# Kernel optimization log

Measured on AMD Instinct MI355X. Metric: run time of the kernel, lower is better.

## Reference

```python
import jax, jax.numpy as jnp
import numpy as np

WIN = (2, 6, 12)            # (vert, lat, lon) window size
P = WIN[0] * WIN[1] * WIN[2]  # 144 patches per window
DIM = 192
HEADS = 6
TYPE_OF_WINDOWS = 4 * 16     # ceil(8/2) * ceil(96/6)
N_WINDOWS = 4 * 16 * 15      # 960 (batch = 1)
BIAS_ROWS = (2 * WIN[2] - 1) * WIN[1] * WIN[1] * WIN[0] * WIN[0]  # 3312


def _construct_index():
    """Replicates EarthAttention3DAbsolute._construct_index in numpy."""
    wz, wh, ww = WIN
    coords_zi = np.arange(wz)
    coords_zj = -np.arange(wz) * wz
    coords_hi = np.arange(wh)
    coords_hj = -np.arange(wh) * wh
    coords_w = np.arange(ww)
    c1 = np.stack(np.meshgrid(coords_zi, coords_hi, coords_w, indexing='ij')).reshape(3, -1)
    c2 = np.stack(np.meshgrid(coords_zj, coords_hj, coords_w, indexing='ij')).reshape(3, -1)
    coords = (c1[:, :, None] - c2[:, None, :]).transpose(1, 2, 0)  # (P, P, 3)
    coords[:, :, 2] += ww - 1
    coords[:, :, 1] *= 2 * ww - 1
    coords[:, :, 0] *= (2 * ww - 1) * wh * wh
    return coords.sum(-1).reshape(-1).astype(np.int32)  # (P*P,)


def setup_inputs() -> dict:
    key = jax.random.key(0)
    ks = jax.random.split(key, 8)
    x = jax.random.normal(ks[0], (N_WINDOWS, P, DIM), dtype=jnp.float32)
    mask = jax.random.normal(ks[1], (N_WINDOWS, P, P), dtype=jnp.float32)
    W_qkv = jax.random.normal(ks[2], (DIM, 3 * DIM), dtype=jnp.float32) * (DIM ** -0.5)
    b_qkv = jax.random.normal(ks[3], (3 * DIM,), dtype=jnp.float32) * 0.02
    W_out = jax.random.normal(ks[4], (DIM, DIM), dtype=jnp.float32) * (DIM ** -0.5)
    b_out = jax.random.normal(ks[5], (DIM,), dtype=jnp.float32) * 0.02
    bias_table = jax.random.normal(ks[6], (BIAS_ROWS, TYPE_OF_WINDOWS, HEADS), dtype=jnp.float32) * 0.02
    position_index = jnp.asarray(_construct_index())
    return {"x": x, "mask": mask, "W_qkv": W_qkv, "b_qkv": b_qkv,
            "W_out": W_out, "b_out": b_out, "bias_table": bias_table,
            "position_index": position_index}


def reference(x, mask, W_qkv, b_qkv, W_out, b_out, bias_table, position_index):
    NW, Pn, C = x.shape            # (960, 144, 192)
    H = HEADS
    D = C // H
    scale = D ** -0.5
    T = bias_table.shape[1]        # type_of_windows

    # QKV projection -> (3, NW, H, P, D)
    qkv = (x @ W_qkv + b_qkv).reshape(NW, Pn, 3, H, D).transpose(2, 0, 3, 1, 4)
    q, k, v = qkv[0] * scale, qkv[1], qkv[2]

    # per-window scores (NW, H, P, P)
    attn = jnp.einsum('whpd,whqd->whpq', q, k)

    # gathered absolute position bias -> (T, H, P, P)
    bias = bias_table[position_index].reshape(Pn, Pn, T, H).transpose(2, 3, 0, 1)
    attn = (attn.reshape(-1, T, H, Pn, Pn) + bias[None]).reshape(NW, H, Pn, Pn)

    # additive shift mask (n_windows, P, P), batch-broadcast
    nwin = mask.shape[0]
    attn = (attn.reshape(NW // nwin, nwin, H, Pn, Pn) + mask[None, :, None]).reshape(NW, H, Pn, Pn)

    attn = jax.nn.softmax(attn, axis=-1)

    out = jnp.einsum('whpq,whqd->wphd', attn, v).reshape(NW, Pn, C)
    return out @ W_out + b_out
```

## Files before the change

### kernel.cpp

```cpp
#include <hip/hip_runtime.h>

#define NWIN   960
#define PP     144
#define CC     192
#define HH     6
#define DD     32
#define TT     64
#define PQ     (PP*PP)
#define MROWS  (NWIN*PP)
#define NQKV   576
#define KT     48
#define QSCALE 0.17677669529663687f


__global__ __launch_bounds__(256) void k0_bias_expand(
    const float* __restrict__ table, const int* __restrict__ pidx,
    float* __restrict__ bias_ws)
{
    int pq = blockIdx.x * 256 + threadIdx.x;
    int idx = pidx[pq];
    const float* row = table + (long)idx * 384;
    for (int th = 0; th < 384; ++th) {
        bias_ws[(unsigned)th * PQ + pq] = row[th];
    }
}

__global__ __launch_bounds__(256) void k2_fused(
    const float* __restrict__ x, const float* __restrict__ Wqkv,
    const float* __restrict__ bqkv, const float* __restrict__ mask,
    const float* __restrict__ bias_ws, float* __restrict__ ao)
{
    __shared__ float Qs[DD][PP + 1];
    __shared__ float Ks[DD][KT + 1];
    __shared__ float Vs[KT][DD];
    __shared__ float UN[6912];

    const int tid = threadIdx.x;
    const int wh = blockIdx.x;
    const int w = wh / HH;
    const int h = wh % HH;
    const int th = (w % TT) * HH + h;
    const float* xw = x + (long)w * PP * CC;
    const float* mb = mask + (long)w * PQ;
    const float* bb = bias_ws + (long)th * PQ;

    const int tp = tid >> 4;
    const int tq = tid & 15;
    const int p0 = tp * 9;
    const int q0 = tq * 3;
    const int d0 = tq * 2;

    {
        float qacc[9][2];
#pragma unroll
        for (int i = 0; i < 9; ++i) { qacc[i][0] = 0.f; qacc[i][1] = 0.f; }

        for (int kc = 0; kc < CC; kc += 32) {
            float* Xs = UN;
            float* Wq = UN + 4752;
            __syncthreads();
            for (int idx = tid; idx < 1152; idx += 256) {
                int p = idx >> 3;
                int cq = (idx & 7) * 4;
                float4 g = *(const float4*)&xw[(long)p * CC + kc + cq];
                Xs[p * 33 + cq + 0] = g.x; Xs[p * 33 + cq + 1] = g.y;
                Xs[p * 33 + cq + 2] = g.z; Xs[p * 33 + cq + 3] = g.w;
            }
            {
                int r = tid >> 3;
                int cq = (tid & 7) * 4;
                float4 g = *(const float4*)&Wqkv[(long)(kc + r) * NQKV + h * DD + cq];
                Wq[r * 33 + cq + 0] = g.x; Wq[r * 33 + cq + 1] = g.y;
                Wq[r * 33 + cq + 2] = g.z; Wq[r * 33 + cq + 3] = g.w;
            }
            __syncthreads();
            for (int c = 0; c < 32; ++c) {
                float b0 = Wq[c * 33 + d0];
                float b1 = Wq[c * 33 + d0 + 1];
                float a[9];
#pragma unroll
                for (int i = 0; i < 9; ++i) a[i] = Xs[(p0 + i) * 33 + c];
#pragma unroll
                for (int i = 0; i < 9; ++i) {
                    qacc[i][0] = fmaf(a[i], b0, qacc[i][0]);
                    qacc[i][1] = fmaf(a[i], b1, qacc[i][1]);
                }
            }
        }
        float bq0 = bqkv[h * DD + d0], bq1 = bqkv[h * DD + d0 + 1];
#pragma unroll
        for (int i = 0; i < 9; ++i) {
            Qs[d0 + 0][p0 + i] = (qacc[i][0] + bq0) * QSCALE;
            Qs[d0 + 1][p0 + i] = (qacc[i][1] + bq1) * QSCALE;
        }
    }

    float O[9][2];
    float mrun[9], lrun[9];
#pragma unroll
    for (int i = 0; i < 9; ++i) {
        O[i][0] = 0.f; O[i][1] = 0.f;
        mrun[i] = -INFINITY; lrun[i] = 0.f;
    }

    const int ty = tid >> 4;
    const int tx = tid & 15;

    for (int kt = 0; kt < 3; ++kt) {
        const int qoff = kt * KT;

        float kv[3][4];
#pragma unroll
        for (int i = 0; i < 3; ++i)
#pragma unroll
            for (int j = 0; j < 4; ++j) kv[i][j] = 0.f;

        for (int kc = 0; kc < CC; kc += 32) {
            float* Xs2 = UN;
            float* Wkv = UN + 1584;
            __syncthreads();
            for (int idx = tid; idx < 384; idx += 256) {
                int r = idx >> 3;
                int cq = (idx & 7) * 4;
                float4 g = *(const float4*)&xw[(long)(qoff + r) * CC + kc + cq];
                Xs2[r * 33 + cq + 0] = g.x; Xs2[r * 33 + cq + 1] = g.y;
                Xs2[r * 33 + cq + 2] = g.z; Xs2[r * 33 + cq + 3] = g.w;
            }
            for (int idx = tid; idx < 512; idx += 256) {
                int r = idx >> 4;
                int q8 = idx & 15;
                int col  = (q8 < 8) ? (192 + h * DD + q8 * 4)
                                    : (384 + h * DD + (q8 - 8) * 4);
                int lcol = q8 * 4;
                float4 g = *(const float4*)&Wqkv[(long)(kc + r) * NQKV + col];
                *(float4*)&Wkv[r * 64 + lcol] = g;
            }
            __syncthreads();
            for (int c = 0; c < 32; ++c) {
                float a2[3];
#pragma unroll
                for (int i = 0; i < 3; ++i) a2[i] = Xs2[(ty * 3 + i) * 33 + c];
                float4 b4 = *(float4*)&Wkv[c * 64 + tx * 4];
#pragma unroll
                for (int i = 0; i < 3; ++i) {
                    kv[i][0] = fmaf(a2[i], b4.x, kv[i][0]);
                    kv[i][1] = fmaf(a2[i], b4.y, kv[i][1]);
                    kv[i][2] = fmaf(a2[i], b4.z, kv[i][2]);
                    kv[i][3] = fmaf(a2[i], b4.w, kv[i][3]);
                }
            }
        }
        __syncthreads();

        if (tx < 8) {
            int dc = tx * 4;
            float4 bk = *(const float4*)&bqkv[192 + h * DD + dc];
#pragma unroll
            for (int i = 0; i < 3; ++i) {
                int r = ty * 3 + i;
                Ks[dc + 0][r] = kv[i][0] + bk.x;
                Ks[dc + 1][r] = kv[i][1] + bk.y;
                Ks[dc + 2][r] = kv[i][2] + bk.z;
                Ks[dc + 3][r] = kv[i][3] + bk.w;
            }
        } else {
            int dc = tx * 4 - 32;
            float4 bv = *(const float4*)&bqkv[384 + h * DD + dc];
#pragma unroll
            for (int i = 0; i < 3; ++i) {
                int r = ty * 3 + i;
                float4 o;
                o.x = kv[i][0] + bv.x; o.y = kv[i][1] + bv.y;
                o.z = kv[i][2] + bv.z; o.w = kv[i][3] + bv.w;
                *(float4*)&Vs[r][dc] = o;
            }
        }
        __syncthreads();

        float acc[9][3];
#pragma unroll
        for (int i = 0; i < 9; ++i)
#pragma unroll
            for (int j = 0; j < 3; ++j) acc[i][j] = 0.f;

        for (int d = 0; d < DD; ++d) {
            float a[9], b[3];
#pragma unroll
            for (int i = 0; i < 9; ++i) a[i] = Qs[d][p0 + i];
#pragma unroll
            for (int j = 0; j < 3; ++j) b[j] = Ks[d][q0 + j];
#pragma unroll
            for (int i = 0; i < 9; ++i)
#pragma unroll
                for (int j = 0; j < 3; ++j) acc[i][j] = fmaf(a[i], b[j], acc[i][j]);
        }

        float* Ps = UN;
        float tmax[9];
#pragma unroll
        for (int i = 0; i < 9; ++i) {
            tmax[i] = -INFINITY;
            int pp = p0 + i;
#pragma unroll
            for (int j = 0; j < 3; ++j) {
                int qq = qoff + q0 + j;
                float s = acc[i][j] + bb[pp * PP + qq] + mb[pp * PP + qq];
                acc[i][j] = s;
                tmax[i] = fmaxf(tmax[i], s);
            }
        }
#pragma unroll
        for (int i = 0; i < 9; ++i) {
#pragma unroll
            for (int off = 1; off < 16; off <<= 1)
                tmax[i] = fmaxf(tmax[i], __shfl_xor(tmax[i], off, 16));
        }
#pragma unroll
        for (int i = 0; i < 9; ++i) {
            float mnew = fmaxf(mrun[i], tmax[i]);
            float scal = __expf(mrun[i] - mnew);
            float psum = 0.f;
#pragma unroll
            for (int j = 0; j < 3; ++j) {
                float p = __expf(acc[i][j] - mnew);
                Ps[(p0 + i) * KT + q0 + j] = p;
                psum += p;
            }
#pragma unroll
            for (int off = 1; off < 16; off <<= 1)
                psum += __shfl_xor(psum, off, 16);
            lrun[i] = lrun[i] * scal + psum;
            O[i][0] *= scal; O[i][1] *= scal;
            mrun[i] = mnew;
        }
        __syncthreads();

        for (int qq = 0; qq < KT; ++qq) {
            float2 v2 = *(const float2*)&Vs[qq][d0];
#pragma unroll
            for (int i = 0; i < 9; ++i) {
                float p = Ps[(p0 + i) * KT + qq];
                O[i][0] = fmaf(p, v2.x, O[i][0]);
                O[i][1] = fmaf(p, v2.y, O[i][1]);
            }
        }
    }

#pragma unroll
    for (int i = 0; i < 9; ++i) {
        float inv = 1.f / lrun[i];
        float2 o2; o2.x = O[i][0] * inv; o2.y = O[i][1] * inv;
        *(float2*)&ao[((long)(w * PP + p0 + i)) * CC + h * DD + d0] = o2;
    }
}

#define BM 128
#define BN 64
#define KC 64
__global__ __launch_bounds__(256) void k3_proj(
    const float* __restrict__ ain, const float* __restrict__ Wout,
    const float* __restrict__ bout, float* __restrict__ out)
{
    __shared__ float As[BM][KC + 1];
    __shared__ float Bs[KC][BN];

    const int tid = threadIdx.x;
    const int rowBase = blockIdx.x * BM;
    const int colBase = blockIdx.y * BN;
    const int r0 = (tid >> 4) * 8;
    const int c0 = (tid & 15) * 4;

    float acc[8][4];
#pragma unroll
    for (int i = 0; i < 8; ++i)
#pragma unroll
        for (int j = 0; j < 4; ++j) acc[i][j] = 0.f;

    for (int kc = 0; kc < CC; kc += KC) {
#pragma unroll
        for (int it = 0; it < 8; ++it) {
            int idx = tid + it * 256;
            int row = idx >> 4;
            int kq  = (idx & 15) * 4;
            float4 g = *(const float4*)&ain[(long)(rowBase + row) * CC + kc + kq];
            As[row][kq + 0] = g.x; As[row][kq + 1] = g.y;
            As[row][kq + 2] = g.z; As[row][kq + 3] = g.w;
        }
#pragma unroll
        for (int it = 0; it < 4; ++it) {
            int idx = tid + it * 256;
            int kk = idx >> 4;
            int n0 = (idx & 15) * 4;
            float4 g = *(const float4*)&Wout[(long)(kc + kk) * CC + colBase + n0];
            *(float4*)&Bs[kk][n0] = g;
        }
        __syncthreads();

        for (int kk = 0; kk < KC; ++kk) {
            float4 b4 = *(const float4*)&Bs[kk][c0];
            float a[8];
#pragma unroll
            for (int i = 0; i < 8; ++i) a[i] = As[r0 + i][kk];
#pragma unroll
            for (int i = 0; i < 8; ++i) {
                acc[i][0] = fmaf(a[i], b4.x, acc[i][0]);
                acc[i][1] = fmaf(a[i], b4.y, acc[i][1]);
                acc[i][2] = fmaf(a[i], b4.z, acc[i][2]);
                acc[i][3] = fmaf(a[i], b4.w, acc[i][3]);
            }
        }
        __syncthreads();
    }

    const int c = colBase + c0;
    float b0 = bout[c], b1 = bout[c + 1], b2 = bout[c + 2], b3 = bout[c + 3];
#pragma unroll
    for (int i = 0; i < 8; ++i) {
        int m = rowBase + r0 + i;
        float4 o;
        o.x = acc[i][0] + b0; o.y = acc[i][1] + b1;
        o.z = acc[i][2] + b2; o.w = acc[i][3] + b3;
        *(float4*)&out[(long)m * CC + c] = o;
    }
}

extern "C" void kernel_launch(void* const* d_in, const int* in_sizes, int n_in,
                              void* d_out, int out_size, void* d_ws, size_t ws_size,
                              hipStream_t stream) {
    const float* x     = (const float*)d_in[0];
    const float* mask  = (const float*)d_in[1];
    const float* Wqkv  = (const float*)d_in[2];
    const float* bqkv  = (const float*)d_in[3];
    const float* Wout  = (const float*)d_in[4];
    const float* bout  = (const float*)d_in[5];
    const float* btab  = (const float*)d_in[6];
    const int*   pidx  = (const int*)d_in[7];
    float* out = (float*)d_out;
    float* ws  = (float*)d_ws;

    float* bws = out;
    float* ao  = ws;

    hipLaunchKernelGGL(k0_bias_expand, dim3(81), dim3(256), 0, stream,
                       btab, pidx, bws);
    hipLaunchKernelGGL(k2_fused, dim3(NWIN * HH), dim3(256), 0, stream,
                       x, Wqkv, bqkv, mask, bws, ao);
    hipLaunchKernelGGL(k3_proj, dim3(MROWS / BM, CC / BN), dim3(256), 0, stream,
                       ao, Wout, bout, out);
}
```

Before: 1.519 ms.

## Rewrite fused attention kernel with split-bf16 MFMA matrix instructions

```diff
diff --git a/kernel.cpp b/kernel.cpp
--- a/kernel.cpp
+++ b/kernel.cpp
@@ -1,4 +1,5 @@
 #include <hip/hip_runtime.h>
+#include <hip/hip_bf16.h>
 
 #define NWIN   960
 #define PP     144
@@ -9,9 +10,54 @@
 #define PQ     (PP*PP)
 #define MROWS  (NWIN*PP)
 #define NQKV   576
-#define KT     48
 #define QSCALE 0.17677669529663687f
 
+using f32x4 = __attribute__((ext_vector_type(4))) float;
+using s16x8 = __attribute__((ext_vector_type(8))) short;
+
+__device__ inline unsigned short f2bf(float x) {
+    __hip_bfloat16 b = __float2bfloat16(x);
+    return *reinterpret_cast<unsigned short*>(&b);
+}
+__device__ inline float bf2f(unsigned short u) {
+    __hip_bfloat16 b = *reinterpret_cast<__hip_bfloat16*>(&u);
+    return __bfloat162float(b);
+}
+__device__ inline unsigned pack_hl(float x) {
+    unsigned short hi = f2bf(x);
+    unsigned short lo = f2bf(x - bf2f(hi));
+    return ((unsigned)lo << 16) | (unsigned)hi;
+}
+
+struct FragHL { s16x8 hi; s16x8 lo; };
+
+__device__ inline FragHL load_frag_hl(const unsigned* base, int row0, int stride) {
+    int lane = threadIdx.x & 63;
+    const unsigned* p = base + (row0 + (lane & 15)) * stride + 8 * (lane >> 4);
+    FragHL f;
+#pragma unroll
+    for (int j = 0; j < 8; ++j) {
+        unsigned u = p[j];
+        f.hi[j] = (short)(u & 0xffffu);
+        f.lo[j] = (short)(u >> 16);
+    }
+    return f;
+}
+__device__ inline s16x8 load_frag_bf(const unsigned short* base, int row0,
+                                     int stride, int koff) {
+    int lane = threadIdx.x & 63;
+    const unsigned short* p = base + (row0 + (lane & 15)) * stride + koff + 8 * (lane >> 4);
+    s16x8 f;
+#pragma unroll
+    for (int j = 0; j < 8; ++j) f[j] = (short)p[j];
+    return f;
+}
+__device__ inline f32x4 mfma3(const FragHL& a, const FragHL& b, f32x4 c) {
+    c = __builtin_amdgcn_mfma_f32_16x16x32_bf16(a.hi, b.hi, c, 0, 0, 0);
+    c = __builtin_amdgcn_mfma_f32_16x16x32_bf16(a.hi, b.lo, c, 0, 0, 0);
+    c = __builtin_amdgcn_mfma_f32_16x16x32_bf16(a.lo, b.hi, c, 0, 0, 0);
+    return c;
+}
 
 __global__ __launch_bounds__(256) void k0_bias_expand(
     const float* __restrict__ table, const int* __restrict__ pidx,
@@ -25,232 +71,194 @@
     }
 }
 
-__global__ __launch_bounds__(256) void k2_fused(
+__global__ __launch_bounds__(256) void k2_mfma(
     const float* __restrict__ x, const float* __restrict__ Wqkv,
     const float* __restrict__ bqkv, const float* __restrict__ mask,
     const float* __restrict__ bias_ws, float* __restrict__ ao)
 {
-    __shared__ float Qs[DD][PP + 1];
-    __shared__ float Ks[DD][KT + 1];
-    __shared__ float Vs[KT][DD];
-    __shared__ float UN[6912];
-
-    const int tid = threadIdx.x;
-    const int wh = blockIdx.x;
-    const int w = wh / HH;
-    const int h = wh % HH;
-    const int th = (w % TT) * HH + h;
+    __shared__ __align__(16) char LDSBUF[63744];
+    unsigned*       Qs = (unsigned*)(LDSBUF);
+    unsigned*       Ks = (unsigned*)(LDSBUF + 20736);
+    unsigned short* Vt = (unsigned short*)(LDSBUF + 41472);
+    unsigned short* Ps = (unsigned short*)(LDSBUF + 52224);
+    unsigned*       Xs = (unsigned*)(LDSBUF);
+    unsigned*       Wt = (unsigned*)(LDSBUF + 20736);
+
+    const int tid  = threadIdx.x;
+    const int lane = tid & 63;
+    const int wv   = tid >> 6;
+    const int bid = blockIdx.x;
+    const int wh  = (bid & 7) * 720 + (bid >> 3);
+    const int w = wh / HH, h = wh % HH;
+    const int thh = (w % TT) * HH + h;
     const float* xw = x + (long)w * PP * CC;
     const float* mb = mask + (long)w * PQ;
-    const float* bb = bias_ws + (long)th * PQ;
-
-    const int tp = tid >> 4;
-    const int tq = tid & 15;
-    const int p0 = tp * 9;
-    const int q0 = tq * 3;
-    const int d0 = tq * 2;
+    const float* bb = bias_ws + (long)thh * PQ;
+
+    const int nmt = (wv == 0) ? 3 : 2;
+    int mts[3];
+    mts[0] = wv; mts[1] = wv + 4; mts[2] = 8;
+
+    const int lgrp = lane >> 4;
+    const int l15  = lane & 15;
+
+    f32x4 acc1[3][6];
+#pragma unroll
+    for (int i = 0; i < 3; ++i)
+#pragma unroll
+        for (int n = 0; n < 6; ++n) acc1[i][n] = f32x4{0.f, 0.f, 0.f, 0.f};
+
+    for (int kc = 0; kc < CC; kc += 32) {
+        __syncthreads();
+        for (int idx = tid; idx < 1152; idx += 256) {
+            int p  = idx >> 3;
+            int c4 = (idx & 7) * 4;
+            float4 g = *(const float4*)&xw[p * CC + kc + c4];
+            unsigned* dst = Xs + p * 36 + c4;
+            dst[0] = pack_hl(g.x); dst[1] = pack_hl(g.y);
+            dst[2] = pack_hl(g.z); dst[3] = pack_hl(g.w);
+        }
+        for (int idx = tid; idx < 768; idx += 256) {
+            int k  = idx / 24;
+            int n4 = (idx % 24) * 4;
+            int seg = n4 >> 5;
+            int gcol = seg * 192 + h * DD + (n4 & 31);
+            float4 g = *(const float4*)&Wqkv[(long)(kc + k) * NQKV + gcol];
+            Wt[(n4 + 0) * 36 + k] = pack_hl(g.x);
+            Wt[(n4 + 1) * 36 + k] = pack_hl(g.y);
+            Wt[(n4 + 2) * 36 + k] = pack_hl(g.z);
+            Wt[(n4 + 3) * 36 + k] = pack_hl(g.w);
+        }
+        __syncthreads();
+        FragHL bfr[6];
+#pragma unroll
+        for (int nt = 0; nt < 6; ++nt) bfr[nt] = load_frag_hl(Wt, nt * 16, 36);
+        for (int im = 0; im < nmt; ++im) {
+            FragHL a = load_frag_hl(Xs, mts[im] * 16, 36);
+#pragma unroll
+            for (int nt = 0; nt < 6; ++nt)
+                acc1[im][nt] = mfma3(a, bfr[nt], acc1[im][nt]);
+        }
+    }
+    __syncthreads();
+
+    for (int im = 0; im < nmt; ++im) {
+        int mrow = mts[im] * 16 + 4 * lgrp;
+#pragma unroll
+        for (int half = 0; half < 2; ++half) {
+            int d = l15 + 16 * half;
+            float bq = bqkv[h * DD + d];
+            float bk = bqkv[192 + h * DD + d];
+            float bv = bqkv[384 + h * DD + d];
+            f32x4 q4 = acc1[im][half];
+            f32x4 k4 = acc1[im][2 + half];
+            f32x4 v4 = acc1[im][4 + half];
+#pragma unroll
+            for (int r = 0; r < 4; ++r) {
+                int row = mrow + r;
+                Qs[row * 36 + d] = pack_hl((q4[r] + bq) * QSCALE);
+                Ks[row * 36 + d] = pack_hl(k4[r] + bk);
+                Vt[d * 168 + row] = f2bf(v4[r] + bv);
+            }
+        }
+    }
+    for (int idx = tid; idx < 512; idx += 256) {
+        int d = idx >> 4;
+        Vt[d * 168 + 144 + (idx & 15)] = 0;
+    }
+    __syncthreads();
+
+    f32x4 sacc[3][9];
+#pragma unroll
+    for (int i = 0; i < 3; ++i)
+#pragma unroll
+        for (int n = 0; n < 9; ++n) sacc[i][n] = f32x4{0.f, 0.f, 0.f, 0.f};
 
     {
-        float qacc[9][2];
-#pragma unroll
-        for (int i = 0; i < 9; ++i) { qacc[i][0] = 0.f; qacc[i][1] = 0.f; }
-
-        for (int kc = 0; kc < CC; kc += 32) {
-            float* Xs = UN;
-            float* Wq = UN + 4752;
-            __syncthreads();
-            for (int idx = tid; idx < 1152; idx += 256) {
-                int p = idx >> 3;
-                int cq = (idx & 7) * 4;
-                float4 g = *(const float4*)&xw[(long)p * CC + kc + cq];
-                Xs[p * 33 + cq + 0] = g.x; Xs[p * 33 + cq + 1] = g.y;
-                Xs[p * 33 + cq + 2] = g.z; Xs[p * 33 + cq + 3] = g.w;
-            }
-            {
-                int r = tid >> 3;
-                int cq = (tid & 7) * 4;
-                float4 g = *(const float4*)&Wqkv[(long)(kc + r) * NQKV + h * DD + cq];
-                Wq[r * 33 + cq + 0] = g.x; Wq[r * 33 + cq + 1] = g.y;
-                Wq[r * 33 + cq + 2] = g.z; Wq[r * 33 + cq + 3] = g.w;
-            }
-            __syncthreads();
-            for (int c = 0; c < 32; ++c) {
-                float b0 = Wq[c * 33 + d0];
-                float b1 = Wq[c * 33 + d0 + 1];
-                float a[9];
-#pragma unroll
-                for (int i = 0; i < 9; ++i) a[i] = Xs[(p0 + i) * 33 + c];
-#pragma unroll
-                for (int i = 0; i < 9; ++i) {
-                    qacc[i][0] = fmaf(a[i], b0, qacc[i][0]);
-                    qacc[i][1] = fmaf(a[i], b1, qacc[i][1]);
+        FragHL aq[3];
+        for (int im = 0; im < nmt; ++im) aq[im] = load_frag_hl(Qs, mts[im] * 16, 36);
+        for (int nt = 0; nt < 9; ++nt) {
+            FragHL b = load_frag_hl(Ks, nt * 16, 36);
+            for (int im = 0; im < nmt; ++im)
+                sacc[im][nt] = mfma3(aq[im], b, sacc[im][nt]);
+        }
+    }
+
+    float rsum[3][4];
+    for (int im = 0; im < nmt; ++im) {
+        int prow = mts[im] * 16 + 4 * lgrp;
+#pragma unroll
+        for (int nt = 0; nt < 9; ++nt) {
+            int qcol = nt * 16 + l15;
+#pragma unroll
+            for (int r = 0; r < 4; ++r)
+                sacc[im][nt][r] += bb[(prow + r) * PP + qcol] + mb[(prow + r) * PP + qcol];
+        }
+#pragma unroll
+        for (int r = 0; r < 4; ++r) {
+            float mx = sacc[im][0][r];
+#pragma unroll
+            for (int nt = 1; nt < 9; ++nt) mx = fmaxf(mx, sacc[im][nt][r]);
+#pragma unroll
+            for (int off = 1; off < 16; off <<= 1)
+                mx = fmaxf(mx, __shfl_xor(mx, off, 16));
+            float sum = 0.f;
+#pragma unroll
+            for (int nt = 0; nt < 9; ++nt) {
+                float e = __expf(sacc[im][nt][r] - mx);
+                sacc[im][nt][r] = e;
+                sum += e;
+            }
+#pragma unroll
+            for (int off = 1; off < 16; off <<= 1)
+                sum += __shfl_xor(sum, off, 16);
+            rsum[im][r] = sum;
+        }
+    }
+
+    f32x4 oacc[3][2];
+#pragma unroll
+    for (int i = 0; i < 3; ++i) { oacc[i][0] = f32x4{0.f,0.f,0.f,0.f};
+                                  oacc[i][1] = f32x4{0.f,0.f,0.f,0.f}; }
+
+    for (int c = 0; c < 5; ++c) {
+        __syncthreads();
+        for (int im = 0; im < nmt; ++im) {
+            int prow = mts[im] * 16 + 4 * lgrp;
+#pragma unroll
+            for (int half = 0; half < 2; ++half) {
+                int nt = 2 * c + half;
+                int col = l15 + 16 * half;
+#pragma unroll
+                for (int r = 0; r < 4; ++r) {
+                    unsigned short v = (nt < 9) ? f2bf(sacc[im][nt][r]) : (unsigned short)0;
+                    Ps[(prow + r) * 40 + col] = v;
                 }
             }
         }
-        float bq0 = bqkv[h * DD + d0], bq1 = bqkv[h * DD + d0 + 1];
-#pragma unroll
-        for (int i = 0; i < 9; ++i) {
-            Qs[d0 + 0][p0 + i] = (qacc[i][0] + bq0) * QSCALE;
-            Qs[d0 + 1][p0 + i] = (qacc[i][1] + bq1) * QSCALE;
-        }
-    }
-
-    float O[9][2];
-    float mrun[9], lrun[9];
-#pragma unroll
-    for (int i = 0; i < 9; ++i) {
-        O[i][0] = 0.f; O[i][1] = 0.f;
-        mrun[i] = -INFINITY; lrun[i] = 0.f;
-    }
-
-    const int ty = tid >> 4;
-    const int tx = tid & 15;
-
-    for (int kt = 0; kt < 3; ++kt) {
-        const int qoff = kt * KT;
-
-        float kv[3][4];
-#pragma unroll
-        for (int i = 0; i < 3; ++i)
-#pragma unroll
-            for (int j = 0; j < 4; ++j) kv[i][j] = 0.f;
-
-        for (int kc = 0; kc < CC; kc += 32) {
-            float* Xs2 = UN;
-            float* Wkv = UN + 1584;
-            __syncthreads();
-            for (int idx = tid; idx < 384; idx += 256) {
-                int r = idx >> 3;
-                int cq = (idx & 7) * 4;
-                float4 g = *(const float4*)&xw[(long)(qoff + r) * CC + kc + cq];
-                Xs2[r * 33 + cq + 0] = g.x; Xs2[r * 33 + cq + 1] = g.y;
-                Xs2[r * 33 + cq + 2] = g.z; Xs2[r * 33 + cq + 3] = g.w;
-            }
-            for (int idx = tid; idx < 512; idx += 256) {
-                int r = idx >> 4;
-                int q8 = idx & 15;
-                int col  = (q8 < 8) ? (192 + h * DD + q8 * 4)
-                                    : (384 + h * DD + (q8 - 8) * 4);
-                int lcol = q8 * 4;
-                float4 g = *(const float4*)&Wqkv[(long)(kc + r) * NQKV + col];
-                *(float4*)&Wkv[r * 64 + lcol] = g;
-            }
-            __syncthreads();
-            for (int c = 0; c < 32; ++c) {
-                float a2[3];
-#pragma unroll
-                for (int i = 0; i < 3; ++i) a2[i] = Xs2[(ty * 3 + i) * 33 + c];
-                float4 b4 = *(float4*)&Wkv[c * 64 + tx * 4];
-#pragma unroll
-                for (int i = 0; i < 3; ++i) {
-                    kv[i][0] = fmaf(a2[i], b4.x, kv[i][0]);
-                    kv[i][1] = fmaf(a2[i], b4.y, kv[i][1]);
-                    kv[i][2] = fmaf(a2[i], b4.z, kv[i][2]);
-                    kv[i][3] = fmaf(a2[i], b4.w, kv[i][3]);
-                }
-            }
-        }
-        __syncthreads();
-
-        if (tx < 8) {
-            int dc = tx * 4;
-            float4 bk = *(const float4*)&bqkv[192 + h * DD + dc];
-#pragma unroll
-            for (int i = 0; i < 3; ++i) {
-                int r = ty * 3 + i;
-                Ks[dc + 0][r] = kv[i][0] + bk.x;
-                Ks[dc + 1][r] = kv[i][1] + bk.y;
-                Ks[dc + 2][r] = kv[i][2] + bk.z;
-                Ks[dc + 3][r] = kv[i][3] + bk.w;
-            }
-        } else {
-            int dc = tx * 4 - 32;
-            float4 bv = *(const float4*)&bqkv[384 + h * DD + dc];
-#pragma unroll
-            for (int i = 0; i < 3; ++i) {
-                int r = ty * 3 + i;
-                float4 o;
-                o.x = kv[i][0] + bv.x; o.y = kv[i][1] + bv.y;
-                o.z = kv[i][2] + bv.z; o.w = kv[i][3] + bv.w;
-                *(float4*)&Vs[r][dc] = o;
-            }
-        }
-        __syncthreads();
-
-        float acc[9][3];
-#pragma unroll
-        for (int i = 0; i < 9; ++i)
-#pragma unroll
-            for (int j = 0; j < 3; ++j) acc[i][j] = 0.f;
-
-        for (int d = 0; d < DD; ++d) {
-            float a[9], b[3];
-#pragma unroll
-            for (int i = 0; i < 9; ++i) a[i] = Qs[d][p0 + i];
-#pragma unroll
-            for (int j = 0; j < 3; ++j) b[j] = Ks[d][q0 + j];
-#pragma unroll
-            for (int i = 0; i < 9; ++i)
-#pragma unroll
-                for (int j = 0; j < 3; ++j) acc[i][j] = fmaf(a[i], b[j], acc[i][j]);
-        }
-
-        float* Ps = UN;
-        float tmax[9];
-#pragma unroll
-        for (int i = 0; i < 9; ++i) {
-            tmax[i] = -INFINITY;
-            int pp = p0 + i;
-#pragma unroll
-            for (int j = 0; j < 3; ++j) {
-                int qq = qoff + q0 + j;
-                float s = acc[i][j] + bb[pp * PP + qq] + mb[pp * PP + qq];
-                acc[i][j] = s;
-                tmax[i] = fmaxf(tmax[i], s);
-            }
-        }
-#pragma unroll
-        for (int i = 0; i < 9; ++i) {
-#pragma unroll
-            for (int off = 1; off < 16; off <<= 1)
-                tmax[i] = fmaxf(tmax[i], __shfl_xor(tmax[i], off, 16));
-        }
-#pragma unroll
-        for (int i = 0; i < 9; ++i) {
-            float mnew = fmaxf(mrun[i], tmax[i]);
-            float scal = __expf(mrun[i] - mnew);
-            float psum = 0.f;
-#pragma unroll
-            for (int j = 0; j < 3; ++j) {
-                float p = __expf(acc[i][j] - mnew);
-                Ps[(p0 + i) * KT + q0 + j] = p;
-                psum += p;
-            }
-#pragma unroll
-            for (int off = 1; off < 16; off <<= 1)
-                psum += __shfl_xor(psum, off, 16);
-            lrun[i] = lrun[i] * scal + psum;
-            O[i][0] *= scal; O[i][1] *= scal;
-            mrun[i] = mnew;
-        }
-        __syncthreads();
-
-        for (int qq = 0; qq < KT; ++qq) {
-            float2 v2 = *(const float2*)&Vs[qq][d0];
-#pragma unroll
-            for (int i = 0; i < 9; ++i) {
-                float p = Ps[(p0 + i) * KT + qq];
-                O[i][0] = fmaf(p, v2.x, O[i][0]);
-                O[i][1] = fmaf(p, v2.y, O[i][1]);
-            }
-        }
-    }
-
-#pragma unroll
-    for (int i = 0; i < 9; ++i) {
-        float inv = 1.f / lrun[i];
-        float2 o2; o2.x = O[i][0] * inv; o2.y = O[i][1] * inv;
-        *(float2*)&ao[((long)(w * PP + p0 + i)) * CC + h * DD + d0] = o2;
+        __syncthreads();
+        for (int im = 0; im < nmt; ++im) {
+            s16x8 a = load_frag_bf(Ps, mts[im] * 16, 40, 0);
+#pragma unroll
+            for (int ntd = 0; ntd < 2; ++ntd) {
+                s16x8 b = load_frag_bf(Vt, ntd * 16, 168, 32 * c);
+                oacc[im][ntd] = __builtin_amdgcn_mfma_f32_16x16x32_bf16(
+                    a, b, oacc[im][ntd], 0, 0, 0);
+            }
+        }
+    }
+
+    for (int im = 0; im < nmt; ++im) {
+        int mrow = mts[im] * 16 + 4 * lgrp;
+#pragma unroll
+        for (int r = 0; r < 4; ++r) {
+            float inv = 1.f / rsum[im][r];
+#pragma unroll
+            for (int ntd = 0; ntd < 2; ++ntd) {
+                int d = l15 + 16 * ntd;
+                ao[((long)(w * PP + mrow + r)) * CC + h * DD + d] = oacc[im][ntd][r] * inv;
+            }
+        }
     }
 }
 
@@ -343,7 +351,7 @@
 
     hipLaunchKernelGGL(k0_bias_expand, dim3(81), dim3(256), 0, stream,
                        btab, pidx, bws);
-    hipLaunchKernelGGL(k2_fused, dim3(NWIN * HH), dim3(256), 0, stream,
+    hipLaunchKernelGGL(k2_mfma, dim3(NWIN * HH), dim3(256), 0, stream,
                        x, Wqkv, bqkv, mask, bws, ao);
     hipLaunchKernelGGL(k3_proj, dim3(MROWS / BM, CC / BN), dim3(256), 0, stream,
                        ao, Wout, bout, out);
```

After: 2.102 ms. 38.4% more time.
